# Optimization experiments

Hardware: AMD Instinct MI355X
Metric: run time of the kernel (lower is better)

## Reference

```python
import jax, jax.numpy as jnp
import numpy as np

N = 50000        # nodes
E = 800000       # edges (before self-loops)
IN = 512         # in_channels
HEADS = 8        # 'head' arg: heads and per-head out dim of conv1
C1 = 8           # per-head channels of conv1 (== head)
OUT = 128        # out_channels of conv2
NEG_SLOPE = 0.2  # PyG GATConv leaky-relu slope


def _glorot(key, shape, fan_in):
    return jax.random.normal(key, shape, jnp.float32) * (1.0 / np.sqrt(fan_in))


def setup_inputs() -> dict:
    key = jax.random.key(0)
    ks = jax.random.split(key, 10)
    x = jax.random.normal(ks[0], (N, IN), jnp.float32)
    edge_index = jax.random.randint(ks[1], (2, E), 0, N, dtype=jnp.int32)
    # conv1: GATConv(IN, C1, heads=HEADS, concat=True)
    W1 = _glorot(ks[2], (IN, HEADS * C1), IN)
    att_src1 = _glorot(ks[3], (HEADS, C1), C1)
    att_dst1 = _glorot(ks[4], (HEADS, C1), C1)
    bias1 = jnp.zeros((HEADS * C1,), jnp.float32)
    # conv2: GATConv(HEADS*C1, OUT, heads=1, concat=False)
    W2 = _glorot(ks[5], (HEADS * C1, OUT), HEADS * C1)
    att_src2 = _glorot(ks[6], (1, OUT), OUT)
    att_dst2 = _glorot(ks[7], (1, OUT), OUT)
    bias2 = jnp.zeros((OUT,), jnp.float32)
    return {"x": x, "edge_index": edge_index,
            "W1": W1, "att_src1": att_src1, "att_dst1": att_dst1, "bias1": bias1,
            "W2": W2, "att_src2": att_src2, "att_dst2": att_dst2, "bias2": bias2}


def gat_conv(x, src, dst, W, a_src, a_dst, bias, heads, concat):
    """PyG GATConv (eval mode, dropout off). src/dst already include self-loops."""
    n = x.shape[0]
    h = (x @ W).reshape(n, heads, -1)                 # [N, H, C]
    s = (h * a_src[None]).sum(-1)                     # [N, H] alpha_src per node
    d = (h * a_dst[None]).sum(-1)                     # [N, H] alpha_dst per node
    alpha = jax.nn.leaky_relu(s[src] + d[dst], NEG_SLOPE)  # [E, H]
    # segment softmax over incoming edges of each destination node
    amax = jax.ops.segment_max(alpha, dst, num_segments=n)  # [N, H]
    amax = jnp.where(jnp.isfinite(amax), amax, 0.0)
    ea = jnp.exp(alpha - amax[dst])                   # [E, H]
    denom = jax.ops.segment_sum(ea, dst, num_segments=n)
    w = ea / (denom[dst] + 1e-16)                     # [E, H]
    msg = h[src] * w[..., None]                       # [E, H, C]
    out = jax.ops.segment_sum(msg, dst, num_segments=n)  # [N, H, C]
    out = out.reshape(n, -1) if concat else out.mean(axis=1)
    return out + bias


def reference(x, edge_index, W1, att_src1, att_dst1, bias1,
              W2, att_src2, att_dst2, bias2):
    n = x.shape[0]
    loop = jnp.arange(n, dtype=edge_index.dtype)      # PyG adds self-loops
    src = jnp.concatenate([edge_index[0], loop])
    dst = jnp.concatenate([edge_index[1], loop])
    h = jax.nn.elu(gat_conv(x, src, dst, W1, att_src1, att_dst1, bias1,
                            heads=HEADS, concat=True))
    out = jax.nn.elu(gat_conv(h, src, dst, W2, att_src2, att_dst2, bias2,
                              heads=1, concat=False))
    return out
```

## Files before the change

### kernel.cpp

```cpp
#include <hip/hip_runtime.h>

#define NEG_SLOPE 0.2f
#define CAP 128

typedef __attribute__((ext_vector_type(8))) short bf16x8;
typedef __attribute__((ext_vector_type(4))) float f32x4;

__device__ __forceinline__ float leaky(float v) {
    return v > 0.0f ? v : NEG_SLOPE * v;
}
__device__ __forceinline__ float elu(float v) {
    return v > 0.0f ? v : (__expf(v) - 1.0f);
}
__device__ __forceinline__ short f2b(float f) {
    return (short)((__float_as_uint(f) + 0x8000u) >> 16);
}
__device__ __forceinline__ float bf2f(unsigned short v) {
    return __uint_as_float(((unsigned)v) << 16);
}

__global__ void prep_k(const float* __restrict__ W1, const float* __restrict__ W2,
                       const float* __restrict__ as2, const float* __restrict__ ad2,
                       unsigned short* __restrict__ w1s, unsigned short* __restrict__ w2s,
                       float* __restrict__ va, float* __restrict__ vd,
                       int* __restrict__ wp, int N) {
    int i = blockIdx.x * 256 + threadIdx.x;
    if (i < N) wp[i] = 0;
    if (i < 64) {
        float sa = 0.f, sd = 0.f;
        for (int n = 0; n < 128; ++n) {
            float w = W2[i * 128 + n];
            sa += w * as2[n];
            sd += w * ad2[n];
        }
        va[i] = sa; vd[i] = sd;
    }
    if (i < 512 * 64) {
        int k = i >> 6, n = i & 63;
        int kt = k >> 5, kk = k & 31;
        int nt = n >> 4, nn = n & 15;
        int lane = (kk >> 3) * 16 + nn, j = kk & 7;
        w1s[(((size_t)(kt * 4 + nt)) * 64 + lane) * 8 + j] = (unsigned short)f2b(W1[i]);
    } else if (i < 512 * 64 + 64 * 128) {
        int i2 = i - 512 * 64;
        int k = i2 >> 7, n = i2 & 127;
        int kt = k >> 5, kk = k & 31;
        int nt = n >> 4, nn = n & 15;
        int lane = (kk >> 3) * 16 + nn, j = kk & 7;
        w2s[(((size_t)(kt * 8 + nt)) * 64 + lane) * 8 + j] = (unsigned short)f2b(W2[i2]);
    }
}

__global__ __launch_bounds__(256) void g1pack_k(const float* __restrict__ X,
                                                const unsigned short* __restrict__ Ws,
                                                const float* __restrict__ Asrc,
                                                const float* __restrict__ Adst,
                                                unsigned short* __restrict__ Hb,
                                                float* __restrict__ S,
                                                float* __restrict__ D,
                                                const int* __restrict__ ei, int E,
                                                int* __restrict__ wp,
                                                int* __restrict__ srcs,
                                                int N, int gblk) {
    if ((int)blockIdx.x >= gblk) {
        int e = ((int)blockIdx.x - gblk) * 256 + threadIdx.x;
        if (e < E) {
            int s = ei[e];
            int d = ei[E + e];
            int c = atomicAdd(&wp[d], 1);
            if (c < CAP) srcs[((size_t)d << 7) + c] = s;
        }
        return;
    }
    const int lane = threadIdx.x & 63;
    const int wave = threadIdx.x >> 6;
    const int m0 = blockIdx.x * 64 + wave * 16;
    const int q = lane >> 4, lc = lane & 15;
    const int arow = m0 + lc;
    const float* xrow = X + (size_t)min(arow, N - 1) * 512 + q * 8;
    const bf16x8* bW = (const bf16x8*)Ws;

    f32x4 acc[4] = {{0.f,0.f,0.f,0.f},{0.f,0.f,0.f,0.f},{0.f,0.f,0.f,0.f},{0.f,0.f,0.f,0.f}};

    for (int g = 0; g < 2; ++g) {
        float4 a[16];
#pragma unroll
        for (int u = 0; u < 16; ++u)
            a[u] = *(const float4*)(xrow + g * 256 + (u >> 1) * 32 + (u & 1) * 4);
#pragma unroll
        for (int u2 = 0; u2 < 8; ++u2) {
            const int kt = g * 8 + u2;
            float4 a0 = a[u2 * 2], a1 = a[u2 * 2 + 1];
            bf16x8 af;
            af[0] = f2b(a0.x); af[1] = f2b(a0.y); af[2] = f2b(a0.z); af[3] = f2b(a0.w);
            af[4] = f2b(a1.x); af[5] = f2b(a1.y); af[6] = f2b(a1.z); af[7] = f2b(a1.w);
#pragma unroll
            for (int nt = 0; nt < 4; ++nt) {
                bf16x8 bf = bW[(size_t)(kt * 4 + nt) * 64 + lane];
                acc[nt] = __builtin_amdgcn_mfma_f32_16x16x32_bf16(af, bf, acc[nt], 0, 0, 0);
            }
        }
    }

    float asc[4], adc[4];
#pragma unroll
    for (int nt = 0; nt < 4; ++nt) { asc[nt] = Asrc[nt * 16 + lc]; adc[nt] = Adst[nt * 16 + lc]; }

#pragma unroll
    for (int r = 0; r < 4; ++r) {
        int row = m0 + q * 4 + r;
        bool ok = row < N;
        if (ok) {
#pragma unroll
            for (int nt = 0; nt < 4; ++nt)
                Hb[(size_t)row * 64 + nt * 16 + lc] = (unsigned short)f2b(acc[nt][r]);
        }
        float ps[4], pd[4];
#pragma unroll
        for (int nt = 0; nt < 4; ++nt) { ps[nt] = acc[nt][r] * asc[nt]; pd[nt] = acc[nt][r] * adc[nt]; }
#pragma unroll
        for (int off = 1; off < 8; off <<= 1) {
#pragma unroll
            for (int nt = 0; nt < 4; ++nt) {
                ps[nt] += __shfl_xor(ps[nt], off);
                pd[nt] += __shfl_xor(pd[nt], off);
            }
        }
        if (ok && !(lc & 7)) {
            int hb = lc >> 3;
#pragma unroll
            for (int nt = 0; nt < 4; ++nt) {
                S[(size_t)row * 8 + nt * 2 + hb] = ps[nt];
                D[(size_t)row * 8 + nt * 2 + hb] = pd[nt];
            }
        }
    }
}

__global__ __launch_bounds__(256) void agg1_k(const int* __restrict__ wp,
                                              const int* __restrict__ srcs,
                                              const float* __restrict__ as1v,
                                              const float* __restrict__ D1,
                                              const unsigned short* __restrict__ H1b,
                                              const float* __restrict__ b1,
                                              const float* __restrict__ va,
                                              const float* __restrict__ vd,
                                              unsigned short* __restrict__ A1b,
                                              float* __restrict__ S2,
                                              float* __restrict__ D2, int N) {
    const int tid  = threadIdx.x;
    const int lane = tid & 63;
    const int wave = tid >> 6;
    const int m0 = blockIdx.x * 16;
    const int h = lane & 7;
    const int eg = lane >> 3;

    float a1c[8], vac[8], vdc[8];
#pragma unroll
    for (int c = 0; c < 8; ++c) {
        a1c[c] = as1v[h * 8 + c];
        vac[c] = va[h * 8 + c];
        vdc[c] = vd[h * 8 + c];
    }

#pragma unroll
    for (int rep = 0; rep < 4; ++rep) {
        const int wid = m0 + wave * 4 + rep;
        if (wid >= N) continue;
        const int deg = min(wp[wid], CAP);
        const size_t b0 = (size_t)wid << 7;
        const float dvh = D1[(size_t)wid * 8 + h];

        float den = 0.0f;
        float acc[8] = {0.f,0.f,0.f,0.f,0.f,0.f,0.f,0.f};
        if (eg == 0) {
            bf16x8 hv = *(const bf16x8*)(H1b + (size_t)wid * 64 + h * 8);
            float hf[8], s = 0.f;
#pragma unroll
            for (int c = 0; c < 8; ++c) { hf[c] = bf2f((unsigned short)hv[c]); s += hf[c] * a1c[c]; }
            float wself = __expf(leaky(s + dvh));
            den = wself;
#pragma unroll
            for (int c = 0; c < 8; ++c) acc[c] = wself * hf[c];
        }

        for (int base = 0; base < deg; base += 8) {
            int i = base + eg;
            bool v = i < deg;
            int src = v ? srcs[b0 + i] : wid;
            bf16x8 hv = *(const bf16x8*)(H1b + (size_t)src * 64 + h * 8);
            float hf[8], s = 0.f;
#pragma unroll
            for (int c = 0; c < 8; ++c) { hf[c] = bf2f((unsigned short)hv[c]); s += hf[c] * a1c[c]; }
            float w = v ? __expf(leaky(s + dvh)) : 0.0f;
            den += w;
#pragma unroll
            for (int c = 0; c < 8; ++c) acc[c] += w * hf[c];
        }
#pragma unroll
        for (int off = 8; off < 64; off <<= 1) {
            den += __shfl_xor(den, off);
#pragma unroll
            for (int c = 0; c < 8; ++c)
                acc[c] += __shfl_xor(acc[c], off);
        }
        const float rden = 1.0f / (den + 1e-16f);
        bf16x8 o;
        float ps = 0.f, pd = 0.f;
#pragma unroll
        for (int c = 0; c < 8; ++c) {
            float fv = elu(acc[c] * rden + b1[h * 8 + c]);
            o[c] = f2b(fv);
            float fr = bf2f((unsigned short)o[c]);
            ps += fr * vac[c];
            pd += fr * vdc[c];
        }
        if (eg == 0)
            *(bf16x8*)(A1b + (size_t)wid * 64 + h * 8) = o;
#pragma unroll
        for (int off = 1; off < 8; off <<= 1) {
            ps += __shfl_xor(ps, off);
            pd += __shfl_xor(pd, off);
        }
        if (lane == 0) { S2[wid] = ps; D2[wid] = pd; }
    }
}

__global__ __launch_bounds__(256) void agg2g2_k(const int* __restrict__ wp,
                                                const int* __restrict__ srcs,
                                                const float* __restrict__ S2,
                                                const float* __restrict__ D2,
                                                const float* __restrict__ va,
                                                const unsigned short* __restrict__ A1b,
                                                const unsigned short* __restrict__ W2s,
                                                const float* __restrict__ b2,
                                                float* __restrict__ out, int N) {
    __shared__ unsigned short sh[16][64];

    const int tid  = threadIdx.x;
    const int lane = tid & 63;
    const int wave = tid >> 6;
    const int m0 = blockIdx.x * 16;
    const int sl = lane & 7;
    const int eg = lane >> 3;

    float vac[8];
#pragma unroll
    for (int c = 0; c < 8; ++c) vac[c] = va[sl * 8 + c];

#pragma unroll
    for (int rep = 0; rep < 4; ++rep) {
        const int nl = wave * 4 + rep;
        const int wid = m0 + nl;
        if (wid < N) {
            const int deg = min(wp[wid], CAP);
            const size_t b0 = (size_t)wid << 7;
            const float dv = D2[wid];

            float den = 0.0f;
            float acc[8] = {0.f,0.f,0.f,0.f,0.f,0.f,0.f,0.f};
            if (eg == 0) {
                const float wself = __expf(leaky(S2[wid] + dv));
                den = wself;
                bf16x8 hv = *(const bf16x8*)(A1b + (size_t)wid * 64 + sl * 8);
#pragma unroll
                for (int c = 0; c < 8; ++c)
                    acc[c] = wself * bf2f((unsigned short)hv[c]);
            }

            for (int base = 0; base < deg; base += 8) {
                int i = base + eg;
                bool v = i < deg;
                int src = v ? srcs[b0 + i] : wid;
                bf16x8 hv = *(const bf16x8*)(A1b + (size_t)src * 64 + sl * 8);
                float hf[8], p = 0.f;
#pragma unroll
                for (int c = 0; c < 8; ++c) { hf[c] = bf2f((unsigned short)hv[c]); p += hf[c] * vac[c]; }
                p += __shfl_xor(p, 1);
                p += __shfl_xor(p, 2);
                p += __shfl_xor(p, 4);
                float w = v ? __expf(leaky(p + dv)) : 0.0f;
                den += w;
#pragma unroll
                for (int c = 0; c < 8; ++c)
                    acc[c] += w * hf[c];
            }
#pragma unroll
            for (int off = 1; off < 64; off <<= 1)
                den += __shfl_xor(den, off);
#pragma unroll
            for (int off = 8; off < 64; off <<= 1) {
#pragma unroll
                for (int c = 0; c < 8; ++c)
                    acc[c] += __shfl_xor(acc[c], off);
            }
            if (eg == 0) {
                const float rden = 1.0f / (den * 0.125f + 1e-16f);
                bf16x8 o;
#pragma unroll
                for (int c = 0; c < 8; ++c)
                    o[c] = f2b(acc[c] * rden);
                *(bf16x8*)(&sh[nl][sl * 8]) = o;
            }
        } else if (eg == 0) {
            *(bf16x8*)(&sh[nl][sl * 8]) = bf16x8{0,0,0,0,0,0,0,0};
        }
    }
    __syncthreads();

    const int q = lane >> 4, lc = lane & 15;
    const bf16x8* bW = (const bf16x8*)W2s;
    const int nt0 = wave * 2;

    f32x4 acc2[2] = {{0.f,0.f,0.f,0.f},{0.f,0.f,0.f,0.f}};
#pragma unroll
    for (int kt = 0; kt < 2; ++kt) {
        bf16x8 af = *(const bf16x8*)(&sh[lc][q * 8 + kt * 32]);
#pragma unroll
        for (int u = 0; u < 2; ++u) {
            bf16x8 bf = bW[(size_t)(kt * 8 + nt0 + u) * 64 + lane];
            acc2[u] = __builtin_amdgcn_mfma_f32_16x16x32_bf16(af, bf, acc2[u], 0, 0, 0);
        }
    }
#pragma unroll
    for (int r = 0; r < 4; ++r) {
        int rl = q * 4 + r;
        int row = m0 + rl;
        if (row < N) {
#pragma unroll
            for (int u = 0; u < 2; ++u) {
                int col = (nt0 + u) * 16 + lc;
                out[(size_t)row * 128 + col] = elu(acc2[u][r] + b2[col]);
            }
        }
    }
}

extern "C" void kernel_launch(void* const* d_in, const int* in_sizes, int n_in,
                              void* d_out, int out_size, void* d_ws, size_t ws_size,
                              hipStream_t stream) {
    const float* x   = (const float*)d_in[0];
    const int*   ei  = (const int*)d_in[1];
    const float* W1  = (const float*)d_in[2];
    const float* as1 = (const float*)d_in[3];
    const float* ad1 = (const float*)d_in[4];
    const float* b1  = (const float*)d_in[5];
    const float* W2  = (const float*)d_in[6];
    const float* as2 = (const float*)d_in[7];
    const float* ad2 = (const float*)d_in[8];
    const float* b2  = (const float*)d_in[9];

    const int N = in_sizes[0] / 512;
    const int E = in_sizes[1] / 2;

    unsigned short* w1s  = (unsigned short*)d_ws;
    unsigned short* w2s  = w1s + 512 * 64;
    unsigned short* h1b  = w2s + 64 * 128;
    unsigned short* a1b  = h1b + (size_t)N * 64;
    float*          s1   = (float*)(a1b + (size_t)N * 64);
    float*          d1   = s1 + (size_t)N * 8;
    float*          s2   = d1 + (size_t)N * 8;
    float*          d2   = s2 + N;
    float*          va   = d2 + N;
    float*          vd   = va + 64;
    int*            wp   = (int*)(vd + 64);
    int*            srcs = wp + N;

    const int B = 256;
    const int gblk  = (N + 63) / 64;
    const int packb = (E + B - 1) / B;
    int prep_n = 512 * 64 + 64 * 128;
    if (N > prep_n) prep_n = N;

    prep_k<<<(prep_n + B - 1) / B, B, 0, stream>>>(W1, W2, as2, ad2, w1s, w2s,
                                                   va, vd, wp, N);
    g1pack_k<<<gblk + packb, B, 0, stream>>>(x, w1s, as1, ad1, h1b, s1, d1,
                                             ei, E, wp, srcs, N, gblk);
    agg1_k<<<(N + 15) / 16, B, 0, stream>>>(wp, srcs, as1, d1, h1b, b1,
                                            va, vd, a1b, s2, d2, N);
    agg2g2_k<<<(N + 15) / 16, B, 0, stream>>>(wp, srcs, s2, d2, va, a1b,
                                              w2s, b2, (float*)d_out, N);
}
```

Baseline: 301.7 us.

## Split GEMM K dimension across waves with LDS reduction in g1pack

Each block now handles 16 rows instead of 64, and its four waves each compute a quarter of the K=512 reduction for all 64 output columns. Partial MFMA accumulators go through shared memory and are summed, then each wave writes one 16-column slice and its per-head attention scores. The aim is more blocks and more parallel memory loads in flight for the bandwidth-bound read of X. The cost is an LDS round trip, a block barrier, and four times as many GEMM blocks, with each block re-reading the whole W1 tile.

```diff
diff --git a/kernel.cpp b/kernel.cpp
--- a/kernel.cpp
+++ b/kernel.cpp
@@ -62,6 +62,7 @@
                                                 int* __restrict__ wp,
                                                 int* __restrict__ srcs,
                                                 int N, int gblk) {
+    __shared__ f32x4 sh[4][4][64];
     if ((int)blockIdx.x >= gblk) {
         int e = ((int)blockIdx.x - gblk) * 256 + threadIdx.x;
         if (e < E) {
@@ -74,7 +75,7 @@
     }
     const int lane = threadIdx.x & 63;
     const int wave = threadIdx.x >> 6;
-    const int m0 = blockIdx.x * 64 + wave * 16;
+    const int m0 = blockIdx.x * 16;
     const int q = lane >> 4, lc = lane & 15;
     const int arow = m0 + lc;
     const float* xrow = X + (size_t)min(arow, N - 1) * 512 + q * 8;
@@ -82,57 +83,56 @@
 
     f32x4 acc[4] = {{0.f,0.f,0.f,0.f},{0.f,0.f,0.f,0.f},{0.f,0.f,0.f,0.f},{0.f,0.f,0.f,0.f}};
 
-    for (int g = 0; g < 2; ++g) {
-        float4 a[16];
-#pragma unroll
-        for (int u = 0; u < 16; ++u)
-            a[u] = *(const float4*)(xrow + g * 256 + (u >> 1) * 32 + (u & 1) * 4);
-#pragma unroll
-        for (int u2 = 0; u2 < 8; ++u2) {
-            const int kt = g * 8 + u2;
-            float4 a0 = a[u2 * 2], a1 = a[u2 * 2 + 1];
-            bf16x8 af;
-            af[0] = f2b(a0.x); af[1] = f2b(a0.y); af[2] = f2b(a0.z); af[3] = f2b(a0.w);
-            af[4] = f2b(a1.x); af[5] = f2b(a1.y); af[6] = f2b(a1.z); af[7] = f2b(a1.w);
-#pragma unroll
-            for (int nt = 0; nt < 4; ++nt) {
-                bf16x8 bf = bW[(size_t)(kt * 4 + nt) * 64 + lane];
-                acc[nt] = __builtin_amdgcn_mfma_f32_16x16x32_bf16(af, bf, acc[nt], 0, 0, 0);
-            }
-        }
-    }
-
-    float asc[4], adc[4];
-#pragma unroll
-    for (int nt = 0; nt < 4; ++nt) { asc[nt] = Asrc[nt * 16 + lc]; adc[nt] = Adst[nt * 16 + lc]; }
-
+    float4 a[8];
+#pragma unroll
+    for (int j = 0; j < 4; ++j) {
+        const int kt = wave * 4 + j;
+        a[j * 2]     = *(const float4*)(xrow + kt * 32);
+        a[j * 2 + 1] = *(const float4*)(xrow + kt * 32 + 4);
+    }
+#pragma unroll
+    for (int j = 0; j < 4; ++j) {
+        const int kt = wave * 4 + j;
+        float4 a0 = a[j * 2], a1 = a[j * 2 + 1];
+        bf16x8 af;
+        af[0] = f2b(a0.x); af[1] = f2b(a0.y); af[2] = f2b(a0.z); af[3] = f2b(a0.w);
+        af[4] = f2b(a1.x); af[5] = f2b(a1.y); af[6] = f2b(a1.z); af[7] = f2b(a1.w);
+#pragma unroll
+        for (int nt = 0; nt < 4; ++nt) {
+            bf16x8 bf = bW[(size_t)(kt * 4 + nt) * 64 + lane];
+            acc[nt] = __builtin_amdgcn_mfma_f32_16x16x32_bf16(af, bf, acc[nt], 0, 0, 0);
+        }
+    }
+
+#pragma unroll
+    for (int nt = 0; nt < 4; ++nt) sh[wave][nt][lane] = acc[nt];
+    __syncthreads();
+
+    f32x4 tot = sh[0][wave][lane];
+    {
+        f32x4 t1 = sh[1][wave][lane];
+        f32x4 t2 = sh[2][wave][lane];
+        f32x4 t3 = sh[3][wave][lane];
+#pragma unroll
+        for (int r = 0; r < 4; ++r) tot[r] = tot[r] + t1[r] + t2[r] + t3[r];
+    }
+    const float asc = Asrc[wave * 16 + lc];
+    const float adc = Adst[wave * 16 + lc];
 #pragma unroll
     for (int r = 0; r < 4; ++r) {
         int row = m0 + q * 4 + r;
         bool ok = row < N;
-        if (ok) {
-#pragma unroll
-            for (int nt = 0; nt < 4; ++nt)
-                Hb[(size_t)row * 64 + nt * 16 + lc] = (unsigned short)f2b(acc[nt][r]);
-        }
-        float ps[4], pd[4];
-#pragma unroll
-        for (int nt = 0; nt < 4; ++nt) { ps[nt] = acc[nt][r] * asc[nt]; pd[nt] = acc[nt][r] * adc[nt]; }
+        if (ok) Hb[(size_t)row * 64 + wave * 16 + lc] = (unsigned short)f2b(tot[r]);
+        float ps = tot[r] * asc, pd = tot[r] * adc;
 #pragma unroll
         for (int off = 1; off < 8; off <<= 1) {
-#pragma unroll
-            for (int nt = 0; nt < 4; ++nt) {
-                ps[nt] += __shfl_xor(ps[nt], off);
-                pd[nt] += __shfl_xor(pd[nt], off);
-            }
+            ps += __shfl_xor(ps, off);
+            pd += __shfl_xor(pd, off);
         }
         if (ok && !(lc & 7)) {
             int hb = lc >> 3;
-#pragma unroll
-            for (int nt = 0; nt < 4; ++nt) {
-                S[(size_t)row * 8 + nt * 2 + hb] = ps[nt];
-                D[(size_t)row * 8 + nt * 2 + hb] = pd[nt];
-            }
+            S[(size_t)row * 8 + wave * 2 + hb] = ps;
+            D[(size_t)row * 8 + wave * 2 + hb] = pd;
         }
     }
 }
@@ -367,7 +367,7 @@
     int*            srcs = wp + N;
 
     const int B = 256;
-    const int gblk  = (N + 63) / 64;
+    const int gblk  = (N + 15) / 16;
     const int packb = (E + B - 1) / B;
     int prep_n = 512 * 64 + 64 * 128;
     if (N > prep_n) prep_n = N;
```

Result: no change. 302.8 us (+0.4%).
